# Kernel tuning notes

Hardware: AMD Instinct MI355X
Metric: run time of the kernel (lower is better)

## Reference

```python
import jax, jax.numpy as jnp
import numpy as np

N_NODES = 200000
N_EDGES = 3200000
VOCAB = 10000
D = 25
EPS = 1e-5


def setup_inputs() -> dict:
    key = jax.random.key(0)
    ks = jax.random.split(key, 16)
    x = jax.random.randint(ks[0], (N_NODES,), 0, VOCAB)
    edge_index = jax.random.randint(ks[1], (2, N_EDGES), 0, N_NODES)
    s = 1.0 / np.sqrt(D)
    inp = {
        'x': x,
        'edge_index': edge_index,
        'emb': jax.random.normal(ks[2], (VOCAB, D), jnp.float32),
        'W1': jax.random.normal(ks[3], (D, D), jnp.float32) * s,
        'b1': jnp.zeros((D,), jnp.float32),
        'g1': jnp.ones((D,), jnp.float32),
        'be1': jnp.zeros((D,), jnp.float32),
        'W2': jax.random.normal(ks[4], (D, D), jnp.float32) * s,
        'b2': jnp.zeros((D,), jnp.float32),
        'g2': jnp.ones((D,), jnp.float32),
        'be2': jnp.zeros((D,), jnp.float32),
        'Wm1': jax.random.normal(ks[5], (D, 12), jnp.float32) * s,
        'bm1': jnp.zeros((12,), jnp.float32),
        'Wm2': jax.random.normal(ks[6], (12, 1), jnp.float32) * (1.0 / np.sqrt(12)),
        'bm2': jnp.zeros((1,), jnp.float32),
    }
    return inp


def gcn_conv(h, src, dst, W, b):
    # PyG GCNConv: h @ W, symmetric normalization with self-loops, scatter-add, + bias
    n = h.shape[0]
    h = h @ W
    loops = jnp.arange(n)
    s = jnp.concatenate([src, loops])  # sources j
    d = jnp.concatenate([dst, loops])  # targets i
    deg = jax.ops.segment_sum(jnp.ones_like(d, h.dtype), d, num_segments=n)
    dinv = jnp.where(deg > 0, jax.lax.rsqrt(jnp.maximum(deg, 1.0)), 0.0)
    norm = dinv[s] * dinv[d]  # [E+N]
    msg = h[s] * norm[:, None]
    out = jax.ops.segment_sum(msg, d, num_segments=n)
    return out + b


def batch_norm(h, g, b):
    mu = jnp.mean(h, axis=0)
    var = jnp.mean((h - mu) ** 2, axis=0)
    return (h - mu) * jax.lax.rsqrt(var + EPS) * g + b


def reference(x, edge_index, emb, W1, b1, g1, be1, W2, b2, g2, be2, Wm1, bm1, Wm2, bm2):
    src, dst = edge_index[0], edge_index[1]
    h = emb[x]  # [N, 25]
    h = jax.nn.relu(batch_norm(gcn_conv(h, src, dst, W1, b1), g1, be1))
    h = jax.nn.relu(batch_norm(gcn_conv(h, src, dst, W2, b2), g2, be2))
    h = jax.nn.relu(h @ Wm1 + bm1)
    return jax.nn.sigmoid(h @ Wm2 + bm2)  # [N, 1]
```

## Files before the change

kernel.cpp:

```cpp
#include <hip/hip_runtime.h>
#include <hip/hip_fp16.h>
#include <math.h>

#define D 25
#define PH_STRIDE 32
#define STATS_BLOCKS 512
#define NBKT 512
#define BSH 9
#define BMSK 511
#define BIN_EDGES 8192
#define SORT_CAP 10240
#define NSLOT 64
#define EPS 1e-5f

__global__ __launch_bounds__(256) void binA(const int* __restrict__ dst,
                                            int* __restrict__ hist2D,
                                            float* __restrict__ stPart, int E) {
    if (blockIdx.x < 25) stPart[blockIdx.x * 256 + threadIdx.x] = 0.0f;
    __shared__ int h[NBKT];
    h[threadIdx.x] = 0;
    h[threadIdx.x + 256] = 0;
    __syncthreads();
    int base = blockIdx.x * BIN_EDGES;
#pragma unroll
    for (int j = 0; j < 32; ++j) {
        int idx = base + j * 256 + threadIdx.x;
        if (idx < E) atomicAdd(&h[dst[idx] >> BSH], 1);
    }
    __syncthreads();
    hist2D[blockIdx.x * NBKT + threadIdx.x] = h[threadIdx.x];
    hist2D[blockIdx.x * NBKT + threadIdx.x + 256] = h[threadIdx.x + 256];
}

__global__ __launch_bounds__(512) void colscan(int* __restrict__ hist2D,
                                               int* __restrict__ bCount, int nbBin) {
    __shared__ int s[512];
    int b = blockIdx.x;
    int j = threadIdx.x;
    int v = (j < nbBin) ? hist2D[j * NBKT + b] : 0;
    s[j] = v;
    __syncthreads();
    for (int off = 1; off < 512; off <<= 1) {
        int x = (j >= off) ? s[j - off] : 0;
        __syncthreads();
        s[j] += x;
        __syncthreads();
    }
    if (j < nbBin) hist2D[j * NBKT + b] = s[j] - v;
    if (j == 0) bCount[b] = s[511];
}

__global__ __launch_bounds__(512) void binB(const int* __restrict__ src,
                                            const int* __restrict__ dst,
                                            const int* __restrict__ hist2D,
                                            const int* __restrict__ bCount,
                                            int* __restrict__ binned, int E) {
    __shared__ int rank[NBKT], basew[NBKT], sc[NBKT];
    int t = threadIdx.x;
    int cnt = bCount[t];
    sc[t] = cnt;
    rank[t] = 0;
    __syncthreads();
    for (int off = 1; off < NBKT; off <<= 1) {
        int x = (t >= off) ? sc[t - off] : 0;
        __syncthreads();
        sc[t] += x;
        __syncthreads();
    }
    basew[t] = (sc[t] - cnt) + hist2D[blockIdx.x * NBKT + t];
    __syncthreads();
    int base = blockIdx.x * BIN_EDGES;
#pragma unroll
    for (int j = 0; j < 16; ++j) {
        int idx = base + j * 512 + t;
        if (idx < E) {
            int d = dst[idx];
            int b = d >> BSH;
            int r = atomicAdd(&rank[b], 1);
            binned[basew[b] + r] = (src[idx] << BSH) | (d & BMSK);
        }
    }
}

__global__ __launch_bounds__(512) void bucket_fill(
        const int* __restrict__ binned, const int* __restrict__ bCount,
        int* __restrict__ degi, int* __restrict__ cursor, int* __restrict__ csr, int N) {
    int b = blockIdx.x;
    int nodeBase = b << BSH;
    if (nodeBase >= N) return;
    __shared__ int h[NBKT];
    __shared__ int s2[512];
    __shared__ int sorted[SORT_CAP];
    int t = threadIdx.x;
    s2[t] = (t < b) ? bCount[t] : 0;
    __syncthreads();
    for (int off = 256; off > 0; off >>= 1) {
        if (t < off) s2[t] += s2[t + off];
        __syncthreads();
    }
    int s = s2[0];
    __syncthreads();
    h[t] = 0;
    __syncthreads();
    int cnt = bCount[b];
    int e = s + cnt;
    for (int k = s + t; k < e; k += 512)
        atomicAdd(&h[binned[k] & BMSK], 1);
    __syncthreads();
    int dg = h[t];
    int node = nodeBase + t;
    if (node < N) degi[node] = dg;
    s2[t] = dg;
    __syncthreads();
    for (int off = 1; off < 512; off <<= 1) {
        int x = (t >= off) ? s2[t - off] : 0;
        __syncthreads();
        s2[t] += x;
        __syncthreads();
    }
    int start = s2[t] - dg;
    h[t] = start;
    if (node < N) cursor[node] = s + s2[t];
    __syncthreads();
    if (cnt <= SORT_CAP) {
        for (int k = s + t; k < e; k += 512) {
            int key = binned[k];
            int p = atomicAdd(&h[key & BMSK], 1);
            sorted[p] = key >> BSH;
        }
        __syncthreads();
        for (int j = t; j < cnt; j += 512)
            csr[s + j] = sorted[j];
    } else {
        for (int k = s + t; k < e; k += 512) {
            int key = binned[k];
            int p = atomicAdd(&h[key & BMSK], 1);
            csr[s + p] = key >> BSH;
        }
    }
}

__global__ __launch_bounds__(256) void embed_gemm1_h(
        const int* __restrict__ x, const float* __restrict__ emb,
        const float* __restrict__ W1, const int* __restrict__ degi,
        __half* __restrict__ Ph, int N) {
    __shared__ float sW[D * D];
    for (int j = threadIdx.x; j < D * D; j += blockDim.x) sW[j] = W1[j];
    __syncthreads();
    int i = blockIdx.x * blockDim.x + threadIdx.x;
    if (i >= N) return;
    const float* er = emb + (size_t)x[i] * D;
    float t[D];
#pragma unroll
    for (int k = 0; k < D; ++k) t[k] = er[k];
    float dinv = rsqrtf((float)degi[i] + 1.0f);
    __half* row = Ph + (size_t)i * PH_STRIDE;
#pragma unroll
    for (int d = 0; d < D; ++d) {
        float acc = 0.0f;
#pragma unroll
        for (int k = 0; k < D; ++k) acc = fmaf(t[k], sW[k * D + d], acc);
        row[d] = __float2half(dinv * acc);
    }
#pragma unroll
    for (int d = D; d < PH_STRIDE; ++d) row[d] = __float2half(0.0f);
}

__global__ __launch_bounds__(256) void gather_stats_w8(
        const int* __restrict__ csr, const int* __restrict__ cursor,
        const int* __restrict__ degi, const __half* __restrict__ Ph,
        const float* __restrict__ bias, __half* __restrict__ Qh,
        float* __restrict__ stPart, int N) {
    int t = threadIdx.x;
    int node = blockIdx.x * 16 + (t >> 4);
    int f = t & 15;
    const __half2* rowb = (const __half2*)Ph;
    float q0 = 0.0f, q1 = 0.0f;
    if (node < N) {
        int end = cursor[node];
        int dg = degi[node];
        int k = end - dg;
        float2 sv = __half22float2(rowb[((size_t)node << 4) + f]);
        float ax = sv.x, ay = sv.y;
        for (; k + 8 <= end; k += 8) {
            int s0 = csr[k],     s1 = csr[k + 1], s2 = csr[k + 2], s3 = csr[k + 3];
            int s4 = csr[k + 4], s5 = csr[k + 5], s6 = csr[k + 6], s7 = csr[k + 7];
            float2 v0 = __half22float2(rowb[((size_t)s0 << 4) + f]);
            float2 v1 = __half22float2(rowb[((size_t)s1 << 4) + f]);
            float2 v2 = __half22float2(rowb[((size_t)s2 << 4) + f]);
            float2 v3 = __half22float2(rowb[((size_t)s3 << 4) + f]);
            float2 v4 = __half22float2(rowb[((size_t)s4 << 4) + f]);
            float2 v5 = __half22float2(rowb[((size_t)s5 << 4) + f]);
            float2 v6 = __half22float2(rowb[((size_t)s6 << 4) + f]);
            float2 v7 = __half22float2(rowb[((size_t)s7 << 4) + f]);
            ax += ((v0.x + v1.x) + (v2.x + v3.x)) + ((v4.x + v5.x) + (v6.x + v7.x));
            ay += ((v0.y + v1.y) + (v2.y + v3.y)) + ((v4.y + v5.y) + (v6.y + v7.y));
        }
        for (; k + 4 <= end; k += 4) {
            int s0 = csr[k], s1 = csr[k + 1], s2 = csr[k + 2], s3 = csr[k + 3];
            float2 v0 = __half22float2(rowb[((size_t)s0 << 4) + f]);
            float2 v1 = __half22float2(rowb[((size_t)s1 << 4) + f]);
            float2 v2 = __half22float2(rowb[((size_t)s2 << 4) + f]);
            float2 v3 = __half22float2(rowb[((size_t)s3 << 4) + f]);
            ax += (v0.x + v1.x) + (v2.x + v3.x);
            ay += (v0.y + v1.y) + (v2.y + v3.y);
        }
        for (; k < end; ++k) {
            float2 v = __half22float2(rowb[((size_t)csr[k] << 4) + f]);
            ax += v.x; ay += v.y;
        }
        float dinv = rsqrtf((float)dg + 1.0f);
        if (f < 13) {
            int j0 = f << 1;
            q0 = fmaf(dinv, ax, bias[j0]);
            if (f < 12) q1 = fmaf(dinv, ay, bias[j0 + 1]);
            ((__half2*)Qh)[((size_t)node << 4) + f] = __floats2half2_rn(q0, q1);
        }
    }
    float ls0 = q0, lq0 = q0 * q0, ls1 = q1, lq1 = q1 * q1;
    ls0 += __shfl_down(ls0, 32, 64); ls0 += __shfl_down(ls0, 16, 64);
    lq0 += __shfl_down(lq0, 32, 64); lq0 += __shfl_down(lq0, 16, 64);
    ls1 += __shfl_down(ls1, 32, 64); ls1 += __shfl_down(ls1, 16, 64);
    lq1 += __shfl_down(lq1, 32, 64); lq1 += __shfl_down(lq1, 16, 64);
    __shared__ float red[4][16][4];
    if ((t & 63) < 16) {
        int w = t >> 6;
        red[w][f][0] = ls0; red[w][f][1] = lq0;
        red[w][f][2] = ls1; red[w][f][3] = lq1;
    }
    __syncthreads();
    if (t < 64) {
        int ff = t >> 2, slot = t & 3;
        float tot = red[0][ff][slot] + red[1][ff][slot] + red[2][ff][slot] + red[3][ff][slot];
        int a = 2 * ff + (slot >> 1);
        if (a < D) atomicAdd(&stPart[(blockIdx.x & (NSLOT - 1)) * 50 + a + (slot & 1) * D], tot);
    }
}

__global__ __launch_bounds__(256) void bn_gemm_hp(
        const __half* __restrict__ Qh, const float* __restrict__ stPart, float invN,
        const float* __restrict__ g, const float* __restrict__ be,
        const float* __restrict__ W, const int* __restrict__ degi,
        __half* __restrict__ Ph, int N) {
    __shared__ float sW[D * D];
    __shared__ float sScale[D], sShift[D];
    __shared__ float sSum[2 * D];
    for (int j = threadIdx.x; j < D * D; j += blockDim.x) sW[j] = W[j];
    if (threadIdx.x < 2 * D) {
        float a = 0.0f;
        for (int k = 0; k < NSLOT; ++k) a += stPart[k * 50 + threadIdx.x];
        sSum[threadIdx.x] = a;
    }
    __syncthreads();
    if (threadIdx.x < D) {
        float m = sSum[threadIdx.x] * invN;
        float v = fmaxf(sSum[D + threadIdx.x] * invN - m * m, 0.0f);
        float sc = rsqrtf(v + EPS) * g[threadIdx.x];
        sScale[threadIdx.x] = sc;
        sShift[threadIdx.x] = be[threadIdx.x] - m * sc;
    }
    __syncthreads();
    int i = blockIdx.x * blockDim.x + threadIdx.x;
    if (i >= N) return;
    const __half2* qrow = (const __half2*)Qh + ((size_t)i << 4);
    float t[D];
#pragma unroll
    for (int ff = 0; ff < 13; ++ff) {
        float2 v = __half22float2(qrow[ff]);
        int j0 = ff << 1;
        t[j0] = fmaxf(0.0f, fmaf(v.x, sScale[j0], sShift[j0]));
        if (ff < 12) t[j0 + 1] = fmaxf(0.0f, fmaf(v.y, sScale[j0 + 1], sShift[j0 + 1]));
    }
    float dinv = rsqrtf((float)degi[i] + 1.0f);
    __half* row = Ph + (size_t)i * PH_STRIDE;
#pragma unroll
    for (int d = 0; d < D; ++d) {
        float acc = 0.0f;
#pragma unroll
        for (int k = 0; k < D; ++k) acc = fmaf(t[k], sW[k * D + d], acc);
        row[d] = __float2half(dinv * acc);
    }
#pragma unroll
    for (int d = D; d < PH_STRIDE; ++d) row[d] = __float2half(0.0f);
}

__global__ __launch_bounds__(256) void final_kernel_p(
        const __half* __restrict__ Qh, const float* __restrict__ stPart, float invN,
        const float* __restrict__ g, const float* __restrict__ be,
        const float* __restrict__ Wm1, const float* __restrict__ bm1,
        const float* __restrict__ Wm2, const float* __restrict__ bm2,
        float* __restrict__ out, int N) {
    __shared__ float sW1[D * 12];
    __shared__ float sb1[12], sW2[12];
    __shared__ float sScale[D], sShift[D];
    __shared__ float sSum[2 * D];
    __shared__ float sb2;
    for (int j = threadIdx.x; j < D * 12; j += blockDim.x) sW1[j] = Wm1[j];
    if (threadIdx.x < 12) {
        sb1[threadIdx.x] = bm1[threadIdx.x];
        sW2[threadIdx.x] = Wm2[threadIdx.x];
    }
    if (threadIdx.x < 2 * D) {
        float a = 0.0f;
        for (int k = 0; k < NSLOT; ++k) a += stPart[k * 50 + threadIdx.x];
        sSum[threadIdx.x] = a;
    }
    if (threadIdx.x == 0) sb2 = bm2[0];
    __syncthreads();
    if (threadIdx.x < D) {
        float m = sSum[threadIdx.x] * invN;
        float v = fmaxf(sSum[D + threadIdx.x] * invN - m * m, 0.0f);
        float sc = rsqrtf(v + EPS) * g[threadIdx.x];
        sScale[threadIdx.x] = sc;
        sShift[threadIdx.x] = be[threadIdx.x] - m * sc;
    }
    __syncthreads();
    int i = blockIdx.x * blockDim.x + threadIdx.x;
    if (i >= N) return;
    const __half2* qrow = (const __half2*)Qh + ((size_t)i << 4);
    float t[D];
#pragma unroll
    for (int ff = 0; ff < 13; ++ff) {
        float2 v = __half22float2(qrow[ff]);
        int j0 = ff << 1;
        t[j0] = fmaxf(0.0f, fmaf(v.x, sScale[j0], sShift[j0]));
        if (ff < 12) t[j0 + 1] = fmaxf(0.0f, fmaf(v.y, sScale[j0 + 1], sShift[j0 + 1]));
    }
    float z = sb2;
#pragma unroll
    for (int j = 0; j < 12; ++j) {
        float m = sb1[j];
#pragma unroll
        for (int k = 0; k < D; ++k) m = fmaf(t[k], sW1[k * 12 + j], m);
        m = fmaxf(0.0f, m);
        z = fmaf(m, sW2[j], z);
    }
    out[i] = 1.0f / (1.0f + expf(-z));
}

__global__ void hist_kernel(const int* __restrict__ dst, int* __restrict__ degi, int E) {
    int e = blockIdx.x * blockDim.x + threadIdx.x;
    if (e < E) atomicAdd(&degi[dst[e]], 1);
}

__global__ __launch_bounds__(256) void embed_gemm1(
        const int* __restrict__ x, const float* __restrict__ emb,
        const float* __restrict__ W1, const int* __restrict__ degi,
        float* __restrict__ P, float* __restrict__ Qdup, int N) {
    __shared__ float sW[D * D];
    for (int j = threadIdx.x; j < D * D; j += blockDim.x) sW[j] = W1[j];
    __syncthreads();
    int i = blockIdx.x * blockDim.x + threadIdx.x;
    if (i >= N) return;
    const float* er = emb + (size_t)x[i] * D;
    float t[D];
#pragma unroll
    for (int k = 0; k < D; ++k) t[k] = er[k];
    float dinv = rsqrtf((float)degi[i] + 1.0f);
#pragma unroll
    for (int d = 0; d < D; ++d) {
        float acc = 0.0f;
#pragma unroll
        for (int k = 0; k < D; ++k) acc = fmaf(t[k], sW[k * D + d], acc);
        float v = dinv * acc;
        P[i * D + d] = v;
        if (Qdup) Qdup[i * D + d] = v;
    }
}

__global__ void scatter_kernel(const int* __restrict__ src, const int* __restrict__ dst,
                               const float* __restrict__ A, float* __restrict__ B, int E) {
    int idx = blockIdx.x * blockDim.x + threadIdx.x;
    int e = idx >> 5;
    int lane = idx & 31;
    if (e >= E || lane >= D) return;
    atomicAdd(&B[dst[e] * D + lane], A[src[e] * D + lane]);
}

__global__ __launch_bounds__(256) void transform_kernel(
        float* __restrict__ Q, const int* __restrict__ degi,
        const float* __restrict__ bias, int N) {
    int i = blockIdx.x * blockDim.x + threadIdx.x;
    if (i >= N) return;
    float dinv = rsqrtf((float)degi[i] + 1.0f);
#pragma unroll
    for (int d = 0; d < D; ++d)
        Q[i * D + d] = fmaf(dinv, Q[i * D + d], bias[d]);
}

__global__ __launch_bounds__(256) void stats_kernel(
        const float* __restrict__ Q, float* __restrict__ st, int N) {
    float ls[D], lq[D];
#pragma unroll
    for (int d = 0; d < D; ++d) { ls[d] = 0.0f; lq[d] = 0.0f; }
    for (int i = blockIdx.x * blockDim.x + threadIdx.x; i < N;
         i += gridDim.x * blockDim.x) {
#pragma unroll
        for (int d = 0; d < D; ++d) {
            float v = Q[i * D + d];
            ls[d] += v;
            lq[d] += v * v;
        }
    }
#pragma unroll
    for (int d = 0; d < D; ++d) {
        for (int off = 32; off > 0; off >>= 1) {
            ls[d] += __shfl_down(ls[d], off, 64);
            lq[d] += __shfl_down(lq[d], off, 64);
        }
    }
    __shared__ float red[4][2 * D];
    int wave = threadIdx.x >> 6;
    int lane = threadIdx.x & 63;
    if (lane == 0) {
#pragma unroll
        for (int d = 0; d < D; ++d) {
            red[wave][d] = ls[d];
            red[wave][D + d] = lq[d];
        }
    }
    __syncthreads();
    if (threadIdx.x < 2 * D) {
        float t = red[0][threadIdx.x] + red[1][threadIdx.x] +
                  red[2][threadIdx.x] + red[3][threadIdx.x];
        atomicAdd(&st[threadIdx.x], t);
    }
}

__global__ __launch_bounds__(256) void bn_gemm(
        const float* __restrict__ Qin, const float* __restrict__ st, float invN,
        const float* __restrict__ g, const float* __restrict__ be,
        const float* __restrict__ W, const int* __restrict__ degi,
        float* __restrict__ P, float* __restrict__ Qdup, int N) {
    __shared__ float sW[D * D];
    __shared__ float sScale[D], sShift[D];
    for (int j = threadIdx.x; j < D * D; j += blockDim.x) sW[j] = W[j];
    if (threadIdx.x < D) {
        float m = st[threadIdx.x] * invN;
        float v = fmaxf(st[D + threadIdx.x] * invN - m * m, 0.0f);
        float sc = rsqrtf(v + EPS) * g[threadIdx.x];
        sScale[threadIdx.x] = sc;
        sShift[threadIdx.x] = be[threadIdx.x] - m * sc;
    }
    __syncthreads();
    int i = blockIdx.x * blockDim.x + threadIdx.x;
    if (i >= N) return;
    float t[D];
#pragma unroll
    for (int d = 0; d < D; ++d)
        t[d] = fmaxf(0.0f, fmaf(Qin[i * D + d], sScale[d], sShift[d]));
    float dinv = rsqrtf((float)degi[i] + 1.0f);
#pragma unroll
    for (int d = 0; d < D; ++d) {
        float acc = 0.0f;
#pragma unroll
        for (int k = 0; k < D; ++k) acc = fmaf(t[k], sW[k * D + d], acc);
        float v = dinv * acc;
        P[i * D + d] = v;
        if (Qdup) Qdup[i * D + d] = v;
    }
}

__global__ __launch_bounds__(256) void final_kernel(
        const float* __restrict__ Q, const float* __restrict__ st, float invN,
        const float* __restrict__ g, const float* __restrict__ be,
        const float* __restrict__ Wm1, const float* __restrict__ bm1,
        const float* __restrict__ Wm2, const float* __restrict__ bm2,
        float* __restrict__ out, int N) {
    __shared__ float sW1[D * 12];
    __shared__ float sb1[12], sW2[12];
    __shared__ float sScale[D], sShift[D];
    __shared__ float sb2;
    for (int j = threadIdx.x; j < D * 12; j += blockDim.x) sW1[j] = Wm1[j];
    if (threadIdx.x < 12) {
        sb1[threadIdx.x] = bm1[threadIdx.x];
        sW2[threadIdx.x] = Wm2[threadIdx.x];
    }
    if (threadIdx.x < D) {
        float m = st[threadIdx.x] * invN;
        float v = fmaxf(st[D + threadIdx.x] * invN - m * m, 0.0f);
        float sc = rsqrtf(v + EPS) * g[threadIdx.x];
        sScale[threadIdx.x] = sc;
        sShift[threadIdx.x] = be[threadIdx.x] - m * sc;
    }
    if (threadIdx.x == 0) sb2 = bm2[0];
    __syncthreads();
    int i = blockIdx.x * blockDim.x + threadIdx.x;
    if (i >= N) return;
    float t[D];
#pragma unroll
    for (int d = 0; d < D; ++d)
        t[d] = fmaxf(0.0f, fmaf(Q[i * D + d], sScale[d], sShift[d]));
    float z = sb2;
#pragma unroll
    for (int j = 0; j < 12; ++j) {
        float m = sb1[j];
#pragma unroll
        for (int k = 0; k < D; ++k) m = fmaf(t[k], sW1[k * 12 + j], m);
        m = fmaxf(0.0f, m);
        z = fmaf(m, sW2[j], z);
    }
    out[i] = 1.0f / (1.0f + expf(-z));
}

extern "C" void kernel_launch(void* const* d_in, const int* in_sizes, int n_in,
                              void* d_out, int out_size, void* d_ws, size_t ws_size,
                              hipStream_t stream) {
    const int*   x    = (const int*)d_in[0];
    const int*   ei   = (const int*)d_in[1];
    const float* emb  = (const float*)d_in[2];
    const float* W1   = (const float*)d_in[3];
    const float* b1   = (const float*)d_in[4];
    const float* g1   = (const float*)d_in[5];
    const float* be1  = (const float*)d_in[6];
    const float* W2   = (const float*)d_in[7];
    const float* b2   = (const float*)d_in[8];
    const float* g2   = (const float*)d_in[9];
    const float* be2  = (const float*)d_in[10];
    const float* Wm1  = (const float*)d_in[11];
    const float* bm1  = (const float*)d_in[12];
    const float* Wm2  = (const float*)d_in[13];
    const float* bm2  = (const float*)d_in[14];
    float* out = (float*)d_out;

    int N = in_sizes[0];
    int E = in_sizes[1] / 2;
    const int* src = ei;
    const int* dst = ei + E;
    float invN = 1.0f / (float)N;

    int nbBin = (E + BIN_EDGES - 1) / BIN_EDGES;
    size_t csrNeed = ((size_t)34 * N + E + 512 + (size_t)nbBin * NBKT + 2 * NSLOT * 50) * 4;
    bool useCSR = (ws_size >= csrNeed) && (N <= NBKT * 512) && (nbBin <= 512) &&
                  ((size_t)E <= (size_t)16 * N) && (nbBin >= 25);

    int nbN  = (N + 255) / 256;
    int nbE  = (E + 255) / 256;
    int nbG  = (N + 15) / 16;
    int nbS  = (int)(((long)E * 32 + 255) / 256);

    if (useCSR) {
        int*    degi    = (int*)d_ws;
        int*    cursor  = degi + N;
        int*    csr     = cursor + N;
        int*    bCount  = csr + E;
        int*    hist2D  = bCount + NBKT;
        __half* Ph      = (__half*)(hist2D + (size_t)nbBin * NBKT);
        __half* Qh      = Ph + (size_t)N * PH_STRIDE;
        float*  stP1    = (float*)(Qh + (size_t)N * PH_STRIDE);
        float*  stP2    = stP1 + NSLOT * 50;
        int*    binned  = (int*)Qh;

        int nbBkt = (N + 511) / 512;

        binA<<<nbBin, 256, 0, stream>>>(dst, hist2D, stP1, E);
        colscan<<<NBKT, 512, 0, stream>>>(hist2D, bCount, nbBin);
        binB<<<nbBin, 512, 0, stream>>>(src, dst, hist2D, bCount, binned, E);
        bucket_fill<<<nbBkt, 512, 0, stream>>>(binned, bCount, degi, cursor, csr, N);
        embed_gemm1_h<<<nbN, 256, 0, stream>>>(x, emb, W1, degi, Ph, N);
        gather_stats_w8<<<nbG, 256, 0, stream>>>(csr, cursor, degi, Ph, b1, Qh, stP1, N);
        bn_gemm_hp<<<nbN, 256, 0, stream>>>(Qh, stP1, invN, g1, be1, W2, degi, Ph, N);
        gather_stats_w8<<<nbG, 256, 0, stream>>>(csr, cursor, degi, Ph, b2, Qh, stP2, N);
        final_kernel_p<<<nbN, 256, 0, stream>>>(Qh, stP2, invN, g2, be2, Wm1, bm1, Wm2, bm2, out, N);
    } else {
        int*   degi  = (int*)d_ws;
        float* P     = (float*)(degi + N);
        float* Q     = P + (size_t)N * D;
        float* stats = Q + (size_t)N * D;
        float* st1 = stats;
        float* st2 = stats + 50;

        hipMemsetAsync(degi, 0, (size_t)N * sizeof(int), stream);
        hipMemsetAsync(stats, 0, 100 * sizeof(float), stream);

        hist_kernel<<<nbE, 256, 0, stream>>>(dst, degi, E);
        embed_gemm1<<<nbN, 256, 0, stream>>>(x, emb, W1, degi, P, Q, N);
        scatter_kernel<<<nbS, 256, 0, stream>>>(src, dst, P, Q, E);
        transform_kernel<<<nbN, 256, 0, stream>>>(Q, degi, b1, N);
        stats_kernel<<<STATS_BLOCKS, 256, 0, stream>>>(Q, st1, N);
        bn_gemm<<<nbN, 256, 0, stream>>>(Q, st1, invN, g1, be1, W2, degi, P, Q, N);
        scatter_kernel<<<nbS, 256, 0, stream>>>(src, dst, P, Q, E);
        transform_kernel<<<nbN, 256, 0, stream>>>(Q, degi, b2, N);
        stats_kernel<<<STATS_BLOCKS, 256, 0, stream>>>(Q, st2, N);
        final_kernel<<<nbN, 256, 0, stream>>>(Q, st2, invN, g2, be2, Wm1, bm1, Wm2, bm2, out, N);
    }
}
```

Measured before the change: 311.8 us.

## Quantize gathered node features to int8 with per-row scale

Stores the pre-aggregation feature rows as 25 int8 values plus a float scale packed into 32 bytes instead of 64-byte fp16 rows. The gather kernel now uses 8 lanes per node, each decoding four int8 values and scaling them by a shuffled row scale, with nontemporal loads of CSR indices and nontemporal stores of the output. The goal is to halve the random-gather traffic that dominates the two aggregation passes. The cost is int8 precision loss in the message values, which may break tolerance, plus extra decode arithmetic and shuffles.

```diff
diff --git a/kernel.cpp b/kernel.cpp
--- a/kernel.cpp
+++ b/kernel.cpp
@@ -3,7 +3,6 @@
 #include <math.h>
 
 #define D 25
-#define PH_STRIDE 32
 #define STATS_BLOCKS 512
 #define NBKT 512
 #define BSH 9
@@ -12,6 +11,9 @@
 #define SORT_CAP 10240
 #define NSLOT 64
 #define EPS 1e-5f
+
+typedef unsigned int u32;
+typedef unsigned long long u64;
 
 __global__ __launch_bounds__(256) void binA(const int* __restrict__ dst,
                                             int* __restrict__ hist2D,
@@ -140,10 +142,44 @@
     }
 }
 
-__global__ __launch_bounds__(256) void embed_gemm1_h(
+
+__device__ __forceinline__ void quant_store_q8(u32* __restrict__ P8, int i,
+                                               const float* v) {
+    float mx = 0.0f;
+#pragma unroll
+    for (int d = 0; d < D; ++d) mx = fmaxf(mx, fabsf(v[d]));
+    float scale = mx * (1.0f / 127.0f);
+    float inv = (mx > 0.0f) ? (127.0f / mx) : 0.0f;
+    u32 w[8];
+#pragma unroll
+    for (int dw = 0; dw < 7; ++dw) {
+        u32 p = 0;
+#pragma unroll
+        for (int j = 0; j < 4; ++j) {
+            int d = dw * 4 + j;
+            int q = (d < D) ? __float2int_rn(v[d] * inv) : 0;
+            p |= ((u32)q & 255u) << (8 * j);
+        }
+        w[dw] = p;
+    }
+    w[7] = __float_as_uint(scale);
+    uint4* o = (uint4*)(P8 + ((size_t)i << 3));
+    o[0] = make_uint4(w[0], w[1], w[2], w[3]);
+    o[1] = make_uint4(w[4], w[5], w[6], w[7]);
+}
+
+__device__ __forceinline__ void acc_q8(u32 w, float c,
+                                       float& a0, float& a1, float& a2, float& a3) {
+    a0 = fmaf(c, (float)((int)(w << 24) >> 24), a0);
+    a1 = fmaf(c, (float)((int)(w << 16) >> 24), a1);
+    a2 = fmaf(c, (float)((int)(w <<  8) >> 24), a2);
+    a3 = fmaf(c, (float)((int)w >> 24), a3);
+}
+
+__global__ __launch_bounds__(256) void embed_gemm1_q8(
         const int* __restrict__ x, const float* __restrict__ emb,
         const float* __restrict__ W1, const int* __restrict__ degi,
-        __half* __restrict__ Ph, int N) {
+        u32* __restrict__ P8, int N) {
     __shared__ float sW[D * D];
     for (int j = threadIdx.x; j < D * D; j += blockDim.x) sW[j] = W1[j];
     __syncthreads();
@@ -154,94 +190,116 @@
 #pragma unroll
     for (int k = 0; k < D; ++k) t[k] = er[k];
     float dinv = rsqrtf((float)degi[i] + 1.0f);
-    __half* row = Ph + (size_t)i * PH_STRIDE;
+    float v[D];
 #pragma unroll
     for (int d = 0; d < D; ++d) {
         float acc = 0.0f;
 #pragma unroll
         for (int k = 0; k < D; ++k) acc = fmaf(t[k], sW[k * D + d], acc);
-        row[d] = __float2half(dinv * acc);
-    }
-#pragma unroll
-    for (int d = D; d < PH_STRIDE; ++d) row[d] = __float2half(0.0f);
-}
-
-__global__ __launch_bounds__(256) void gather_stats_w8(
+        v[d] = dinv * acc;
+    }
+    quant_store_q8(P8, i, v);
+}
+
+__global__ __launch_bounds__(256) void gather_stats_q8(
         const int* __restrict__ csr, const int* __restrict__ cursor,
-        const int* __restrict__ degi, const __half* __restrict__ Ph,
+        const int* __restrict__ degi, const u32* __restrict__ P8,
         const float* __restrict__ bias, __half* __restrict__ Qh,
         float* __restrict__ stPart, int N) {
+    __shared__ float red[4][8][8];
     int t = threadIdx.x;
-    int node = blockIdx.x * 16 + (t >> 4);
-    int f = t & 15;
-    const __half2* rowb = (const __half2*)Ph;
-    float q0 = 0.0f, q1 = 0.0f;
+    int node = blockIdx.x * 32 + (t >> 3);
+    int f = t & 7;
+    float a0 = 0.f, a1 = 0.f, a2 = 0.f, a3 = 0.f;
+    float q0 = 0.f, q1 = 0.f, q2 = 0.f, q3 = 0.f;
     if (node < N) {
         int end = cursor[node];
-        int dg = degi[node];
+        int dg  = degi[node];
         int k = end - dg;
-        float2 sv = __half22float2(rowb[((size_t)node << 4) + f]);
-        float ax = sv.x, ay = sv.y;
+        u32 wsf = P8[((size_t)node << 3) + f];
+        float csf = __shfl(__uint_as_float(wsf), 7, 8);
+        acc_q8(wsf, csf, a0, a1, a2, a3);
         for (; k + 8 <= end; k += 8) {
-            int s0 = csr[k],     s1 = csr[k + 1], s2 = csr[k + 2], s3 = csr[k + 3];
-            int s4 = csr[k + 4], s5 = csr[k + 5], s6 = csr[k + 6], s7 = csr[k + 7];
-            float2 v0 = __half22float2(rowb[((size_t)s0 << 4) + f]);
-            float2 v1 = __half22float2(rowb[((size_t)s1 << 4) + f]);
-            float2 v2 = __half22float2(rowb[((size_t)s2 << 4) + f]);
-            float2 v3 = __half22float2(rowb[((size_t)s3 << 4) + f]);
-            float2 v4 = __half22float2(rowb[((size_t)s4 << 4) + f]);
-            float2 v5 = __half22float2(rowb[((size_t)s5 << 4) + f]);
-            float2 v6 = __half22float2(rowb[((size_t)s6 << 4) + f]);
-            float2 v7 = __half22float2(rowb[((size_t)s7 << 4) + f]);
-            ax += ((v0.x + v1.x) + (v2.x + v3.x)) + ((v4.x + v5.x) + (v6.x + v7.x));
-            ay += ((v0.y + v1.y) + (v2.y + v3.y)) + ((v4.y + v5.y) + (v6.y + v7.y));
-        }
-        for (; k + 4 <= end; k += 4) {
-            int s0 = csr[k], s1 = csr[k + 1], s2 = csr[k + 2], s3 = csr[k + 3];
-            float2 v0 = __half22float2(rowb[((size_t)s0 << 4) + f]);
-            float2 v1 = __half22float2(rowb[((size_t)s1 << 4) + f]);
-            float2 v2 = __half22float2(rowb[((size_t)s2 << 4) + f]);
-            float2 v3 = __half22float2(rowb[((size_t)s3 << 4) + f]);
-            ax += (v0.x + v1.x) + (v2.x + v3.x);
-            ay += (v0.y + v1.y) + (v2.y + v3.y);
+            int e0 = __builtin_nontemporal_load(csr + k);
+            int e1 = __builtin_nontemporal_load(csr + k + 1);
+            int e2 = __builtin_nontemporal_load(csr + k + 2);
+            int e3 = __builtin_nontemporal_load(csr + k + 3);
+            int e4 = __builtin_nontemporal_load(csr + k + 4);
+            int e5 = __builtin_nontemporal_load(csr + k + 5);
+            int e6 = __builtin_nontemporal_load(csr + k + 6);
+            int e7 = __builtin_nontemporal_load(csr + k + 7);
+            u32 w0 = P8[((size_t)e0 << 3) + f];
+            u32 w1 = P8[((size_t)e1 << 3) + f];
+            u32 w2 = P8[((size_t)e2 << 3) + f];
+            u32 w3 = P8[((size_t)e3 << 3) + f];
+            u32 w4 = P8[((size_t)e4 << 3) + f];
+            u32 w5 = P8[((size_t)e5 << 3) + f];
+            u32 w6 = P8[((size_t)e6 << 3) + f];
+            u32 w7 = P8[((size_t)e7 << 3) + f];
+            float c0 = __shfl(__uint_as_float(w0), 7, 8);
+            float c1 = __shfl(__uint_as_float(w1), 7, 8);
+            float c2 = __shfl(__uint_as_float(w2), 7, 8);
+            float c3 = __shfl(__uint_as_float(w3), 7, 8);
+            float c4 = __shfl(__uint_as_float(w4), 7, 8);
+            float c5 = __shfl(__uint_as_float(w5), 7, 8);
+            float c6 = __shfl(__uint_as_float(w6), 7, 8);
+            float c7 = __shfl(__uint_as_float(w7), 7, 8);
+            acc_q8(w0, c0, a0, a1, a2, a3);
+            acc_q8(w1, c1, a0, a1, a2, a3);
+            acc_q8(w2, c2, a0, a1, a2, a3);
+            acc_q8(w3, c3, a0, a1, a2, a3);
+            acc_q8(w4, c4, a0, a1, a2, a3);
+            acc_q8(w5, c5, a0, a1, a2, a3);
+            acc_q8(w6, c6, a0, a1, a2, a3);
+            acc_q8(w7, c7, a0, a1, a2, a3);
         }
         for (; k < end; ++k) {
-            float2 v = __half22float2(rowb[((size_t)csr[k] << 4) + f]);
-            ax += v.x; ay += v.y;
+            int e = __builtin_nontemporal_load(csr + k);
+            u32 w = P8[((size_t)e << 3) + f];
+            float c = __shfl(__uint_as_float(w), 7, 8);
+            acc_q8(w, c, a0, a1, a2, a3);
         }
         float dinv = rsqrtf((float)dg + 1.0f);
-        if (f < 13) {
-            int j0 = f << 1;
-            q0 = fmaf(dinv, ax, bias[j0]);
-            if (f < 12) q1 = fmaf(dinv, ay, bias[j0 + 1]);
-            ((__half2*)Qh)[((size_t)node << 4) + f] = __floats2half2_rn(q0, q1);
-        }
-    }
-    float ls0 = q0, lq0 = q0 * q0, ls1 = q1, lq1 = q1 * q1;
-    ls0 += __shfl_down(ls0, 32, 64); ls0 += __shfl_down(ls0, 16, 64);
-    lq0 += __shfl_down(lq0, 32, 64); lq0 += __shfl_down(lq0, 16, 64);
-    ls1 += __shfl_down(ls1, 32, 64); ls1 += __shfl_down(ls1, 16, 64);
-    lq1 += __shfl_down(lq1, 32, 64); lq1 += __shfl_down(lq1, 16, 64);
-    __shared__ float red[4][16][4];
-    if ((t & 63) < 16) {
-        int w = t >> 6;
-        red[w][f][0] = ls0; red[w][f][1] = lq0;
-        red[w][f][2] = ls1; red[w][f][3] = lq1;
+        int j0 = f << 2;
+        if (f < 7) {
+            q0 = fmaf(dinv, a0, bias[j0]);
+            if (j0 + 1 < D) q1 = fmaf(dinv, a1, bias[j0 + 1]);
+            if (j0 + 2 < D) q2 = fmaf(dinv, a2, bias[j0 + 2]);
+            if (j0 + 3 < D) q3 = fmaf(dinv, a3, bias[j0 + 3]);
+        }
+        __half2 h01 = __floats2half2_rn(q0, q1);
+        __half2 h23 = __floats2half2_rn(q2, q3);
+        union { __half2 h[2]; u64 u; } cv;
+        cv.h[0] = h01; cv.h[1] = h23;
+        __builtin_nontemporal_store(cv.u, (u64*)Qh + ((size_t)node << 3) + f);
+    }
+    float r[8] = {q0, q1, q2, q3, q0 * q0, q1 * q1, q2 * q2, q3 * q3};
+#pragma unroll
+    for (int v = 0; v < 8; ++v) {
+        r[v] += __shfl_down(r[v], 32, 64);
+        r[v] += __shfl_down(r[v], 16, 64);
+        r[v] += __shfl_down(r[v], 8, 64);
+    }
+    int wv = t >> 6;
+    if ((t & 63) < 8) {
+#pragma unroll
+        for (int v = 0; v < 8; ++v) red[wv][f][v] = r[v];
     }
     __syncthreads();
     if (t < 64) {
-        int ff = t >> 2, slot = t & 3;
-        float tot = red[0][ff][slot] + red[1][ff][slot] + red[2][ff][slot] + red[3][ff][slot];
-        int a = 2 * ff + (slot >> 1);
-        if (a < D) atomicAdd(&stPart[(blockIdx.x & (NSLOT - 1)) * 50 + a + (slot & 1) * D], tot);
-    }
-}
-
-__global__ __launch_bounds__(256) void bn_gemm_hp(
+        int ff = t >> 3, v = t & 7;
+        float tot = red[0][ff][v] + red[1][ff][v] + red[2][ff][v] + red[3][ff][v];
+        int a = (ff << 2) + (v & 3);
+        if (a < D)
+            atomicAdd(&stPart[(blockIdx.x & (NSLOT - 1)) * 50 + (v >> 2) * D + a], tot);
+    }
+}
+
+__global__ __launch_bounds__(256) void bn_gemm_q8(
         const __half* __restrict__ Qh, const float* __restrict__ stPart, float invN,
         const float* __restrict__ g, const float* __restrict__ be,
         const float* __restrict__ W, const int* __restrict__ degi,
-        __half* __restrict__ Ph, int N) {
+        u32* __restrict__ P8, int N) {
     __shared__ float sW[D * D];
     __shared__ float sScale[D], sShift[D];
     __shared__ float sSum[2 * D];
@@ -272,16 +330,15 @@
         if (ff < 12) t[j0 + 1] = fmaxf(0.0f, fmaf(v.y, sScale[j0 + 1], sShift[j0 + 1]));
     }
     float dinv = rsqrtf((float)degi[i] + 1.0f);
-    __half* row = Ph + (size_t)i * PH_STRIDE;
+    float vout[D];
 #pragma unroll
     for (int d = 0; d < D; ++d) {
         float acc = 0.0f;
 #pragma unroll
         for (int k = 0; k < D; ++k) acc = fmaf(t[k], sW[k * D + d], acc);
-        row[d] = __float2half(dinv * acc);
-    }
-#pragma unroll
-    for (int d = D; d < PH_STRIDE; ++d) row[d] = __float2half(0.0f);
+        vout[d] = dinv * acc;
+    }
+    quant_store_q8(P8, i, vout);
 }
 
 __global__ __launch_bounds__(256) void final_kernel_p(
@@ -530,13 +587,14 @@
     float invN = 1.0f / (float)N;
 
     int nbBin = (E + BIN_EDGES - 1) / BIN_EDGES;
-    size_t csrNeed = ((size_t)34 * N + E + 512 + (size_t)nbBin * NBKT + 2 * NSLOT * 50) * 4;
+    size_t csrNeed = ((size_t)26 * N + E + 512 + (size_t)nbBin * NBKT +
+                      2 * NSLOT * 50 + 16) * 4;
     bool useCSR = (ws_size >= csrNeed) && (N <= NBKT * 512) && (nbBin <= 512) &&
                   ((size_t)E <= (size_t)16 * N) && (nbBin >= 25);
 
     int nbN  = (N + 255) / 256;
     int nbE  = (E + 255) / 256;
-    int nbG  = (N + 15) / 16;
+    int nbG  = (N + 31) / 32;
     int nbS  = (int)(((long)E * 32 + 255) / 256);
 
     if (useCSR) {
@@ -545,9 +603,10 @@
         int*    csr     = cursor + N;
         int*    bCount  = csr + E;
         int*    hist2D  = bCount + NBKT;
-        __half* Ph      = (__half*)(hist2D + (size_t)nbBin * NBKT);
-        __half* Qh      = Ph + (size_t)N * PH_STRIDE;
-        float*  stP1    = (float*)(Qh + (size_t)N * PH_STRIDE);
+        int*    hEnd    = hist2D + (size_t)nbBin * NBKT;
+        u32*    P8      = (u32*)(((uintptr_t)hEnd + 15) & ~(uintptr_t)15);
+        __half* Qh      = (__half*)(P8 + 8 * (size_t)N);
+        float*  stP1    = (float*)((u32*)Qh + 16 * (size_t)N);
         float*  stP2    = stP1 + NSLOT * 50;
         int*    binned  = (int*)Qh;
 
@@ -557,10 +616,10 @@
         colscan<<<NBKT, 512, 0, stream>>>(hist2D, bCount, nbBin);
         binB<<<nbBin, 512, 0, stream>>>(src, dst, hist2D, bCount, binned, E);
         bucket_fill<<<nbBkt, 512, 0, stream>>>(binned, bCount, degi, cursor, csr, N);
-        embed_gemm1_h<<<nbN, 256, 0, stream>>>(x, emb, W1, degi, Ph, N);
-        gather_stats_w8<<<nbG, 256, 0, stream>>>(csr, cursor, degi, Ph, b1, Qh, stP1, N);
-        bn_gemm_hp<<<nbN, 256, 0, stream>>>(Qh, stP1, invN, g1, be1, W2, degi, Ph, N);
-        gather_stats_w8<<<nbG, 256, 0, stream>>>(csr, cursor, degi, Ph, b2, Qh, stP2, N);
+        embed_gemm1_q8<<<nbN, 256, 0, stream>>>(x, emb, W1, degi, P8, N);
+        gather_stats_q8<<<nbG, 256, 0, stream>>>(csr, cursor, degi, P8, b1, Qh, stP1, N);
+        bn_gemm_q8<<<nbN, 256, 0, stream>>>(Qh, stP1, invN, g1, be1, W2, degi, P8, N);
+        gather_stats_q8<<<nbG, 256, 0, stream>>>(csr, cursor, degi, P8, b2, Qh, stP2, N);
         final_kernel_p<<<nbN, 256, 0, stream>>>(Qh, stP2, invN, g2, be2, Wm1, bm1, Wm2, bm2, out, N);
     } else {
         int*   degi  = (int*)d_ws;
```

After: 298.4 us. 1.04x faster.
